# Kernel optimization log

Hardware: AMD Instinct MI355X
Metric: run time of the kernel (lower is better)

## Reference

```python
import jax, jax.numpy as jnp
import numpy as np

L, C, H = 4, 512, 8
HD = C // H

def silu(x):
    return x * jax.nn.sigmoid(x)

def layernorm(x, g, b, eps=1e-5):
    m = x.mean(-1, keepdims=True)
    v = ((x - m) ** 2).mean(-1, keepdims=True)
    return (x - m) * jax.lax.rsqrt(v + eps) * g + b

def adaln(x, t, w, b):
    # x: (N,B,C), t: (B,C), w: (2C,C), b: (2C,)
    mod = silu(t) @ w.T + b
    scale, shift = jnp.split(mod, 2, axis=-1)
    return x * (1.0 + scale[None]) + shift[None]

def embed_rotary(x, pos):
    # x: (B,N,C), pos: (B,N,C,2) with [...,0]=cos, [...,1]=sin
    cos, sin = pos[..., 0], pos[..., 1]
    x2 = jnp.stack([-x[..., 1::2], x[..., 0::2]], axis=-1).reshape(x.shape)
    return x * cos + x2 * sin

def setup_inputs() -> dict:
    key = jax.random.key(0)
    ks = jax.random.split(key, 24)
    Nq, Nkv, B = 1024, 2048, 4
    query = jax.random.normal(ks[0], (Nq, B, C), jnp.float32)
    value = jax.random.normal(ks[1], (Nkv, B, C), jnp.float32)
    diff_ts = jax.random.normal(ks[2], (B, C), jnp.float32)
    # valid rotary codes: cos/sin of random angles
    aq = jax.random.uniform(ks[3], (B, Nq, C), jnp.float32, 0.0, 2 * np.pi)
    ak = jax.random.uniform(ks[4], (B, Nkv, C), jnp.float32, 0.0, 2 * np.pi)
    query_pos = jnp.stack([jnp.cos(aq), jnp.sin(aq)], axis=-1)
    value_pos = jnp.stack([jnp.cos(ak), jnp.sin(ak)], axis=-1)
    s = 0.02
    inp = dict(query=query, value=value, diff_ts=diff_ts,
               query_pos=query_pos, value_pos=value_pos,
               aw_attn=jax.random.normal(ks[5], (L, 2 * C, C)) * s,
               ab_attn=jax.random.normal(ks[6], (L, 2 * C)) * s,
               in_w=jax.random.normal(ks[7], (L, 3 * C, C)) * s,
               in_b=jnp.zeros((L, 3 * C)),
               out_w=jax.random.normal(ks[8], (L, C, C)) * s,
               out_b=jnp.zeros((L, C)),
               ln1_g=jnp.ones((L, C)), ln1_b=jnp.zeros((L, C)),
               aw_ffn=jax.random.normal(ks[9], (L, 2 * C, C)) * s,
               ab_ffn=jax.random.normal(ks[10], (L, 2 * C)) * s,
               w1=jax.random.normal(ks[11], (L, C, C)) * s,
               b1=jnp.zeros((L, C)),
               w2=jax.random.normal(ks[12], (L, C, C)) * s,
               b2=jnp.zeros((L, C)),
               ln2_g=jnp.ones((L, C)), ln2_b=jnp.zeros((L, C)))
    return inp

def _forward(query, value, diff_ts, query_pos, value_pos,
             aw_attn, ab_attn, in_w, in_b, out_w, out_b, ln1_g, ln1_b,
             aw_ffn, ab_ffn, w1, b1, w2, b2, ln2_g, ln2_b):
    Nq, B, _ = query.shape
    Nkv = value.shape[0]
    scaling = HD ** -0.5
    outputs = []
    q = query
    for i in range(L):
        # --- cross-attention layer ---
        aq = adaln(q, diff_ts, aw_attn[i], ab_attn[i])
        wq, wk, wv = jnp.split(in_w[i], 3, axis=0)
        bq, bk, bv = jnp.split(in_b[i], 3, axis=0)
        qp = (aq @ wq.T + bq) * scaling          # (Nq,B,C)
        kp = value @ wk.T + bk                    # (Nkv,B,C)
        vp = value @ wv.T + bv
        qb = embed_rotary(qp.transpose(1, 0, 2), query_pos)  # (B,Nq,C)
        kb = embed_rotary(kp.transpose(1, 0, 2), value_pos)  # (B,Nkv,C)
        vb = vp.transpose(1, 0, 2)
        qh = qb.reshape(B, Nq, H, HD).transpose(0, 2, 1, 3)   # (B,H,Nq,HD)
        kh = kb.reshape(B, Nkv, H, HD).transpose(0, 2, 1, 3)
        vh = vb.reshape(B, Nkv, H, HD).transpose(0, 2, 1, 3)
        scores = jnp.einsum('bhqd,bhkd->bhqk', qh, kh)
        attn = jax.nn.softmax(scores, axis=-1)
        o = jnp.einsum('bhqk,bhkd->bhqd', attn, vh)
        o = o.transpose(0, 2, 1, 3).reshape(B, Nq, C).transpose(1, 0, 2)  # (Nq,B,C)
        o = o @ out_w[i].T + out_b[i]
        q = layernorm(q + o, ln1_g[i], ln1_b[i])
        # --- feedforward layer (residual uses AdaLN-modulated x) ---
        xa = adaln(q, diff_ts, aw_ffn[i], ab_ffn[i])
        h = jax.nn.relu(xa @ w1[i].T + b1[i])
        h = h @ w2[i].T + b2[i]
        q = layernorm(xa + h, ln2_g[i], ln2_b[i])
        outputs.append(q)
    return jnp.stack(outputs)  # (L, Nq, B, C)

def reference(query, value, diff_ts, query_pos, value_pos,
              aw_attn, ab_attn, in_w, in_b, out_w, out_b, ln1_g, ln1_b,
              aw_ffn, ab_ffn, w1, b1, w2, b2, ln2_g, ln2_b):
    return _forward(query, value, diff_ts, query_pos, value_pos,
                    aw_attn, ab_attn, in_w, in_b, out_w, out_b, ln1_g, ln1_b,
                    aw_ffn, ab_ffn, w1, b1, w2, b2, ln2_g, ln2_b)
```

## Files before the change

### kernel.cpp

```cpp
#include <hip/hip_runtime.h>
#include <hip/hip_bf16.h>

typedef __hip_bfloat16 bf16;
typedef __attribute__((ext_vector_type(8))) short short8;
typedef __attribute__((ext_vector_type(4))) short s16x4;
typedef __attribute__((ext_vector_type(4))) float f32x4;

#define CDIM 512
#define BDIM 4
#define HDIM 8
#define HDQ  64
#define NQ   1024
#define NKV  2048
#define LAYERS 4
#define SPLIT 2

#if defined(__has_builtin)
#if __has_builtin(__builtin_amdgcn_global_load_lds)
#define USE_GLL 1
#endif
#endif

static __device__ __forceinline__ short f2s(float f) {
    bf16 h = __float2bfloat16(f);
    return *reinterpret_cast<short*>(&h);
}


__global__ __launch_bounds__(256) void convall_k(
    const float* __restrict__ s0, const float* __restrict__ s1,
    const float* __restrict__ s2, const float* __restrict__ s3,
    const float* __restrict__ s4,
    bf16* __restrict__ d0, bf16* __restrict__ d1, bf16* __restrict__ d2,
    bf16* __restrict__ d3, bf16* __restrict__ d4) {
    int gid = blockIdx.x * 256 + threadIdx.x;
    const float* src; bf16* dst; int off;
    if (gid < 1048576)      { src = s0; dst = d0; off = gid; }
    else if (gid < 1835008) { src = s1; dst = d1; off = gid - 1048576; }
    else if (gid < 2097152) { src = s2; dst = d2; off = gid - 1835008; }
    else if (gid < 2359296) { src = s3; dst = d3; off = gid - 2097152; }
    else                    { src = s4; dst = d4; off = gid - 2359296; }
    f32x4 v = *(const f32x4*)(src + (size_t)off * 4);
    s16x4 o;
    o[0] = f2s(v[0]); o[1] = f2s(v[1]); o[2] = f2s(v[2]); o[3] = f2s(v[3]);
    *(s16x4*)(dst + (size_t)off * 4) = o;
}

__global__ __launch_bounds__(256) void modall_k(const float* __restrict__ diff_ts,
    const float* __restrict__ aw_attn, const float* __restrict__ ab_attn,
    const float* __restrict__ aw_ffn,  const float* __restrict__ ab_ffn,
    float* __restrict__ mod) {
    int wv = blockIdx.x * 4 + (threadIdx.x >> 6);
    int lane = threadIdx.x & 63;
    int col  = wv & 1023;
    int b    = (wv >> 10) & 3;
    int kind = (wv >> 12) & 1;
    int l    = wv >> 13;
    const float* w = (kind ? aw_ffn : aw_attn) + ((size_t)l * 1024 + col) * CDIM + lane * 8;
    const float* tb = diff_ts + b * CDIM + lane * 8;
    f32x4 w0 = *(const f32x4*)w;
    f32x4 w1 = *(const f32x4*)(w + 4);
    f32x4 t0 = *(const f32x4*)tb;
    f32x4 t1 = *(const f32x4*)(tb + 4);
    #pragma unroll
    for (int j = 0; j < 4; ++j) {
        t0[j] = t0[j] / (1.f + __expf(-t0[j]));
        t1[j] = t1[j] / (1.f + __expf(-t1[j]));
    }
    f32x4 pp = w0 * t0 + w1 * t1;
    float acc = (pp[0] + pp[1]) + (pp[2] + pp[3]);
    #pragma unroll
    for (int off = 32; off; off >>= 1) acc += __shfl_xor(acc, off);
    if (lane == 0)
        mod[wv] = acc + (kind ? ab_ffn : ab_attn)[l * 1024 + col];
}

__global__ __launch_bounds__(256) void adaln_k(const float* __restrict__ x,
                                               const float* __restrict__ mod,
                                               bf16* __restrict__ outb) {
    int i = blockIdx.x * 256 + threadIdx.x;
    int c = i & 511;
    int b = (i >> 9) & 3;
    outb[i] = __float2bfloat16(x[i] * (1.f + mod[b * 1024 + c]) + mod[b * 1024 + 512 + c]);
}

__global__ __launch_bounds__(256) void ln_ad_k(const float* __restrict__ x,
                                               const float* __restrict__ res,
                                               const float* __restrict__ g,
                                               const float* __restrict__ bb,
                                               const float* __restrict__ mod,
                                               float* __restrict__ ln_f,
                                               float* __restrict__ ln_f2,
                                               float* __restrict__ ad_f,
                                               bf16* __restrict__ ad_b) {
    int row = blockIdx.x;
    int t = threadIdx.x;
    size_t base = (size_t)row * CDIM;
    float v0 = x[base + t] + res[base + t];
    float v1 = x[base + t + 256] + res[base + t + 256];
    float s1 = v0 + v1;
    float s2 = v0 * v0 + v1 * v1;
    #pragma unroll
    for (int off = 32; off; off >>= 1) {
        s1 += __shfl_xor(s1, off);
        s2 += __shfl_xor(s2, off);
    }
    __shared__ float a1[4], a2[4];
    int w = t >> 6;
    if ((t & 63) == 0) { a1[w] = s1; a2[w] = s2; }
    __syncthreads();
    s1 = a1[0] + a1[1] + a1[2] + a1[3];
    s2 = a2[0] + a2[1] + a2[2] + a2[3];
    float mean = s1 * (1.f / 512.f);
    float var = s2 * (1.f / 512.f) - mean * mean;
    float rs = rsqrtf(var + 1e-5f);
    float y0 = (v0 - mean) * rs * g[t] + bb[t];
    float y1 = (v1 - mean) * rs * g[t + 256] + bb[t + 256];
    if (ln_f)  { ln_f[base + t] = y0;  ln_f[base + t + 256] = y1; }
    if (ln_f2) { ln_f2[base + t] = y0; ln_f2[base + t + 256] = y1; }
    if (mod) {
        int b = row & 3;
        float o0 = y0 * (1.f + mod[b * 1024 + t]) + mod[b * 1024 + 512 + t];
        float o1 = y1 * (1.f + mod[b * 1024 + t + 256]) + mod[b * 1024 + 512 + t + 256];
        if (ad_f) { ad_f[base + t] = o0; ad_f[base + t + 256] = o1; }
        ad_b[base + t] = __float2bfloat16(o0);
        ad_b[base + t + 256] = __float2bfloat16(o1);
    }
}

template <int EPI, int WM, int NT>
__global__ __launch_bounds__(256) void mgemm_k(
    const bf16* __restrict__ A, const bf16* __restrict__ Wt,
    const float* __restrict__ bias, void* __restrict__ out0v,
    void* __restrict__ out1v, int M, int N, int K,
    const float* __restrict__ pos, float scl, int Nseq) {
    __shared__ bf16 As[2][2][64 * 32];
    __shared__ bf16 Bs[2][2][64 * 32];
    int t = threadIdx.x;
    int w = t >> 6;
    int lane = t & 63;
    int l16 = lane & 15;
    int quad = lane >> 4;
    int wy = w >> 1, wx = w & 1;
    int bm = blockIdx.y * 64;
    int bn = blockIdx.x * 64;
    int lr2 = lane >> 2;
    int lc4 = lane & 3;

    f32x4 acc[WM][NT] = {};

    auto stage = [&](int buf, int k0) {
#if USE_GLL
        const bf16* sa = A + (size_t)(bm + w * 16 + lr2) * K + k0 + lc4 * 8;
        const bf16* sb = Wt + (size_t)(bn + w * 16 + lr2) * K + k0 + lc4 * 8;
        #pragma unroll
        for (int j = 0; j < 2; ++j) {
            __builtin_amdgcn_global_load_lds(
                (const unsigned int __attribute__((address_space(1)))*)(sa + j * 32),
                (unsigned int __attribute__((address_space(3)))*)(&As[buf][j][w * 512]),
                16, 0, 0);
            __builtin_amdgcn_global_load_lds(
                (const unsigned int __attribute__((address_space(1)))*)(sb + j * 32),
                (unsigned int __attribute__((address_space(3)))*)(&Bs[buf][j][w * 512]),
                16, 0, 0);
        }
#else
        for (int e = t; e < 512; e += 256) {
            int sub = e >> 8, c = e & 255;
            int row = c >> 2, c4 = c & 3;
            *(uint4*)&As[buf][sub][row * 32 + c4 * 8] =
                *(const uint4*)(A + (size_t)(bm + row) * K + k0 + sub * 32 + c4 * 8);
            *(uint4*)&Bs[buf][sub][row * 32 + c4 * 8] =
                *(const uint4*)(Wt + (size_t)(bn + row) * K + k0 + sub * 32 + c4 * 8);
        }
#endif
    };

    stage(0, 0);
    __syncthreads();
    int cur = 0;

    for (int k0 = 0; k0 < K; k0 += 64) {
        if (k0 + 64 < K) stage(cur ^ 1, k0 + 64);

        #pragma unroll
        for (int kk = 0; kk < 2; ++kk) {
            short8 af[WM], bfr[NT];
            #pragma unroll
            for (int mt = 0; mt < WM; ++mt)
                af[mt] = *(const short8*)
                    &As[cur][kk][((wy * WM + mt) * 16 + l16) * 32 + quad * 8];
            #pragma unroll
            for (int nt = 0; nt < NT; ++nt)
                bfr[nt] = *(const short8*)
                    &Bs[cur][kk][((wx * NT + nt) * 16 + l16) * 32 + quad * 8];
            #pragma unroll
            for (int mt = 0; mt < WM; ++mt)
                #pragma unroll
                for (int nt = 0; nt < NT; ++nt)
                    acc[mt][nt] = __builtin_amdgcn_mfma_f32_16x16x32_bf16(
                        af[mt], bfr[nt], acc[mt][nt], 0, 0, 0);
        }

        __syncthreads();
        cur ^= 1;
    }

    #pragma unroll
    for (int nt = 0; nt < NT; ++nt) {
        int n = bn + (wx * NT + nt) * 16 + l16;
        float bnv = (EPI == 4) ? 0.f : bias[n];
        #pragma unroll
        for (int mt = 0; mt < WM; ++mt) {
            #pragma unroll
            for (int r = 0; r < 4; ++r) {
                int m = bm + (wy * WM + mt) * 16 + quad * 4 + r;
                float v = acc[mt][nt][r] + ((EPI == 4) ? bias[m] : bnv);
                if (EPI == 0) {
                    ((float*)out0v)[(size_t)m * N + n] = v;
                } else if (EPI == 1) {
                    ((bf16*)out0v)[(size_t)m * N + n] = __float2bfloat16(fmaxf(v, 0.f));
                } else if (EPI == 4) {
                    int hh = m >> 6, dd = m & 63;
                    int bsel = n & 3, key = n >> 2;
                    ((bf16*)out0v)[((size_t)(bsel * HDIM + hh) * HDQ + dd) * NKV + key] =
                        __float2bfloat16(v);
                } else {
                    v *= scl;
                    int c = n;
                    int nseq = m >> 2, b = m & 3;
                    float part = __shfl_xor(v, 1);
                    const float* pp = pos + (((size_t)b * Nseq + nseq) * CDIM + c) * 2;
                    float cs = pp[0], sn = pp[1];
                    float o = (l16 & 1) ? (v * cs + part * sn) : (v * cs - part * sn);
                    bf16* op = (bf16*)out0v +
                               ((size_t)(b * HDIM + (c >> 6)) * Nseq + nseq) * HDQ + (c & 63);
                    *op = __float2bfloat16(o);
                }
            }
        }
    }
}

__global__ __launch_bounds__(256) void attn4_k(const bf16* __restrict__ qh,
                                               const bf16* __restrict__ kh,
                                               const bf16* __restrict__ vT,
                                               float* __restrict__ pl,
                                               float* __restrict__ pacc) {
    __shared__ short Kb[2][64 * 64];
    __shared__ short Vb[2][64 * 64];
    __shared__ short Ps[4][16 * 64];
    int t = threadIdx.x;
    int wave = t >> 6, lane = t & 63;
    int l16 = lane & 15, quad = lane >> 4;
    int bh = blockIdx.y;
    int q0 = blockIdx.x * 64 + wave * 16;
    int kbase = blockIdx.z * (NKV / SPLIT);

    const bf16* qbase = qh + ((size_t)bh * NQ + q0) * HDQ;
    short8 aq0 = *(const short8*)(qbase + (size_t)l16 * HDQ + quad * 8);
    short8 aq1 = *(const short8*)(qbase + (size_t)l16 * HDQ + 32 + quad * 8);
    const bf16* kbh = kh + ((size_t)bh * NKV + kbase) * HDQ;
    const bf16* vbh = vT + (size_t)bh * HDQ * NKV + kbase;

    int r0 = wave * 16;
    int lr = lane >> 3;
    int swz_src = ((lane & 7) ^ lr) * 8;

    auto stage = [&](int buf, int kt) {
#if USE_GLL
        #pragma unroll
        for (int j = 0; j < 2; ++j) {
            int rr = r0 + j * 8;
            __builtin_amdgcn_global_load_lds(
                (const unsigned int __attribute__((address_space(1)))*)
                    (kbh + (size_t)(kt + rr + lr) * HDQ + swz_src),
                (unsigned int __attribute__((address_space(3)))*)&Kb[buf][rr * 64],
                16, 0, 0);
            __builtin_amdgcn_global_load_lds(
                (const unsigned int __attribute__((address_space(1)))*)
                    (vbh + (size_t)(rr + lr) * NKV + kt + swz_src),
                (unsigned int __attribute__((address_space(3)))*)&Vb[buf][rr * 64],
                16, 0, 0);
        }
#else
        #pragma unroll
        for (int j = 0; j < 2; ++j) {
            int rr = r0 + j * 8 + lr;
            int lc = lane & 7;
            *(short8*)&Kb[buf][rr * 64 + ((lc ^ (rr & 7)) * 8)] =
                *(const short8*)(kbh + (size_t)(kt + rr) * HDQ + lc * 8);
            *(short8*)&Vb[buf][rr * 64 + ((lc ^ (rr & 7)) * 8)] =
                *(const short8*)(vbh + (size_t)rr * NKV + kt + lc * 8);
        }
#endif
    };

    f32x4 accO[4] = {};
    float lsum[4] = {0.f, 0.f, 0.f, 0.f};

    stage(0, 0);
    __syncthreads();
    int cur = 0;
    int swz_m = l16 & 7;

    for (int kt = 0; kt < NKV / SPLIT; kt += 64) {
        if (kt + 64 < NKV / SPLIT) stage(cur ^ 1, kt + 64);

        f32x4 sc[4] = {};
        #pragma unroll
        for (int nt = 0; nt < 4; ++nt) {
            const short* kr = &Kb[cur][(nt * 16 + l16) * 64];
            short8 bk0 = *(const short8*)&kr[(quad ^ swz_m) * 8];
            short8 bk1 = *(const short8*)&kr[((quad + 4) ^ swz_m) * 8];
            sc[nt] = __builtin_amdgcn_mfma_f32_16x16x32_bf16(aq0, bk0, sc[nt], 0, 0, 0);
            sc[nt] = __builtin_amdgcn_mfma_f32_16x16x32_bf16(aq1, bk1, sc[nt], 0, 0, 0);
        }

        #pragma unroll
        for (int r = 0; r < 4; ++r) {
            float p0 = exp2f(sc[0][r]);
            float p1 = exp2f(sc[1][r]);
            float p2 = exp2f(sc[2][r]);
            float p3 = exp2f(sc[3][r]);
            lsum[r] += (p0 + p1) + (p2 + p3);
            int pr = quad * 4 + r;
            short* prow = &Ps[wave][pr * 64];
            int pm = pr & 7;
            int ch = l16 >> 3, kl = l16 & 7;
            prow[((ch ^ pm) << 3) + kl]       = f2s(p0);
            prow[(((ch + 2) ^ pm) << 3) + kl] = f2s(p1);
            prow[(((ch + 4) ^ pm) << 3) + kl] = f2s(p2);
            prow[(((ch + 6) ^ pm) << 3) + kl] = f2s(p3);
        }

        const short* prd = &Ps[wave][l16 * 64];
        short8 pa0 = *(const short8*)&prd[(quad ^ swz_m) * 8];
        short8 pa1 = *(const short8*)&prd[((quad + 4) ^ swz_m) * 8];
        #pragma unroll
        for (int nt = 0; nt < 4; ++nt) {
            const short* vr = &Vb[cur][(nt * 16 + l16) * 64];
            short8 bv0 = *(const short8*)&vr[(quad ^ swz_m) * 8];
            short8 bv1 = *(const short8*)&vr[((quad + 4) ^ swz_m) * 8];
            accO[nt] = __builtin_amdgcn_mfma_f32_16x16x32_bf16(pa0, bv0, accO[nt], 0, 0, 0);
            accO[nt] = __builtin_amdgcn_mfma_f32_16x16x32_bf16(pa1, bv1, accO[nt], 0, 0, 0);
        }

        __syncthreads();
        cur ^= 1;
    }

    #pragma unroll
    for (int r = 0; r < 4; ++r) {
        #pragma unroll
        for (int off = 1; off < 16; off <<= 1) lsum[r] += __shfl_xor(lsum[r], off);
    }

    size_t rowbase = ((size_t)blockIdx.z * 32 + bh) * NQ + q0;
    #pragma unroll
    for (int r = 0; r < 4; ++r) {
        size_t row = rowbase + quad * 4 + r;
        if (l16 == 0) pl[row] = lsum[r];
        #pragma unroll
        for (int nt = 0; nt < 4; ++nt)
            pacc[row * 64 + nt * 16 + l16] = accO[nt][r];
    }
}

__global__ __launch_bounds__(256) void attn_comb_k(const float* __restrict__ pl,
                                                   const float* __restrict__ pacc,
                                                   bf16* __restrict__ o) {
    int idx = blockIdx.x * 256 + threadIdx.x;
    int d = idx & 63;
    int row = idx >> 6;
    int q = row & (NQ - 1);
    int bh = row >> 10;
    const int S = 32 * NQ;
    float l = pl[row] + pl[S + row];
    float v = pacc[(size_t)row * 64 + d] + pacc[(size_t)(S + row) * 64 + d];
    int b = bh >> 3, h = bh & 7;
    o[((size_t)(q * BDIM + b)) * CDIM + h * HDQ + d] = __float2bfloat16(v / l);
}


extern "C" void kernel_launch(void* const* d_in, const int* in_sizes, int n_in,
                              void* d_out, int out_size, void* d_ws, size_t ws_size,
                              hipStream_t stream) {
    const float* query     = (const float*)d_in[0];
    const float* value     = (const float*)d_in[1];
    const float* diff_ts   = (const float*)d_in[2];
    const float* query_pos = (const float*)d_in[3];
    const float* value_pos = (const float*)d_in[4];
    const float* aw_attn   = (const float*)d_in[5];
    const float* ab_attn   = (const float*)d_in[6];
    const float* in_w      = (const float*)d_in[7];
    const float* in_b      = (const float*)d_in[8];
    const float* out_w     = (const float*)d_in[9];
    const float* out_b     = (const float*)d_in[10];
    const float* ln1_g     = (const float*)d_in[11];
    const float* ln1_b     = (const float*)d_in[12];
    const float* aw_ffn    = (const float*)d_in[13];
    const float* ab_ffn    = (const float*)d_in[14];
    const float* w1        = (const float*)d_in[15];
    const float* b1        = (const float*)d_in[16];
    const float* w2        = (const float*)d_in[17];
    const float* b2        = (const float*)d_in[18];
    const float* ln2_g     = (const float*)d_in[19];
    const float* ln2_b     = (const float*)d_in[20];
    float* out_f = (float*)d_out;

    float* ws      = (float*)d_ws;
    float* mod_ws  = ws + 2048;
    float* q_cur   = ws + 34816;
    float* buf_a   = q_cur + 2097152;
    float* buf_p   = buf_a + 2097152;
    bf16* a_bf     = (bf16*)(buf_p + 2097152);
    bf16* h_bf     = a_bf + 2097152;
    bf16* qh       = h_bf + 2097152;
    bf16* kh       = qh + 2097152;
    bf16* vt       = kh + 4194304;
    bf16* val_bf   = vt + 4194304;
    bf16* winb     = val_bf + 4194304;
    bf16* woutb    = winb + 3145728;
    bf16* w1b      = woutb + 1048576;
    bf16* w2b      = w1b + 1048576;
    float* pacc    = buf_a;
    float* pl      = (float*)a_bf;

    const int MQ = NQ * BDIM;
    const int MKV = NKV * BDIM;
    const float scaling = 0.125f * 1.44269504f;

    modall_k<<<8192, 256, 0, stream>>>(diff_ts, aw_attn, ab_attn, aw_ffn, ab_ffn, mod_ws);
    convall_k<<<10240, 256, 0, stream>>>(value, in_w, out_w, w1, w2,
                                         val_bf, winb, woutb, w1b, w2b);
    adaln_k<<<(MQ * CDIM) / 256, 256, 0, stream>>>(query, mod_ws, a_bf);

    for (int i = 0; i < LAYERS; ++i) {
        const float* mod_ffn  = mod_ws + i * 8192 + 4096;
        const float* mod_attn_next = (i + 1 < LAYERS) ? (mod_ws + (i + 1) * 8192) : nullptr;
        const bf16* winb_i = winb + (size_t)i * 1536 * CDIM;
        const float* in_b_i = in_b + (size_t)i * 1536;
        const float* qsrc = (i == 0) ? query : q_cur;

        mgemm_k<2, 2, 2><<<dim3(8, MQ / 64), 256, 0, stream>>>(
            a_bf, winb_i, in_b_i, qh, nullptr, MQ, 512, CDIM, query_pos, scaling, NQ);
        mgemm_k<2, 2, 2><<<dim3(8, MKV / 64), 256, 0, stream>>>(
            val_bf, winb_i + (size_t)512 * CDIM, in_b_i + 512, kh, nullptr, MKV, 512,
            CDIM, value_pos, 1.f, NKV);
        mgemm_k<4, 2, 2><<<dim3(MKV / 64, 8), 256, 0, stream>>>(
            winb_i + (size_t)1024 * CDIM, val_bf, in_b_i + 1024, vt, nullptr,
            512, MKV, CDIM, nullptr, 0.f, 0);
        attn4_k<<<dim3(NQ / 64, BDIM * HDIM, SPLIT), 256, 0, stream>>>(
            qh, kh, vt, pl, pacc);
        attn_comb_k<<<8192, 256, 0, stream>>>(pl, pacc, h_bf);
        mgemm_k<0, 2, 2><<<dim3(8, MQ / 64), 256, 0, stream>>>(
            h_bf, woutb + (size_t)i * CDIM * CDIM, out_b + i * CDIM, buf_p, nullptr,
            MQ, 512, CDIM, nullptr, 0.f, 0);
        ln_ad_k<<<MQ, 256, 0, stream>>>(qsrc, buf_p, ln1_g + i * CDIM, ln1_b + i * CDIM,
                                        mod_ffn, nullptr, nullptr, buf_a, a_bf);
        mgemm_k<1, 2, 2><<<dim3(8, MQ / 64), 256, 0, stream>>>(
            a_bf, w1b + (size_t)i * CDIM * CDIM, b1 + i * CDIM, h_bf, nullptr,
            MQ, 512, CDIM, nullptr, 0.f, 0);
        mgemm_k<0, 2, 2><<<dim3(8, MQ / 64), 256, 0, stream>>>(
            h_bf, w2b + (size_t)i * CDIM * CDIM, b2 + i * CDIM, buf_p, nullptr,
            MQ, 512, CDIM, nullptr, 0.f, 0);
        ln_ad_k<<<MQ, 256, 0, stream>>>(buf_a, buf_p, ln2_g + i * CDIM, ln2_b + i * CDIM,
                                        mod_attn_next, q_cur,
                                        out_f + (size_t)i * MQ * CDIM, nullptr, a_bf);
    }
}
```

Measured before the change: 701.5 us.

## Merge QKV projections into one launch, split-K small GEMMs, remap attention grid

The three Q/K/V projection GEMMs become one kernel that picks its section from the block index, which removes two launches and fills the GPU with one larger grid. The out-projection and FFN2 GEMMs are split along K into two partial outputs, doubling the block count for these 512-block GEMMs. The partial sums are added inside the following layernorm kernel. The attention grid is flattened and its block ids permuted, plausibly to spread work across XCDs and improve cache locality. The split-K costs an extra fp32 partial buffer write and read.

```diff
diff --git a/kernel.cpp b/kernel.cpp
--- a/kernel.cpp
+++ b/kernel.cpp
@@ -86,6 +86,7 @@
 
 __global__ __launch_bounds__(256) void ln_ad_k(const float* __restrict__ x,
                                                const float* __restrict__ res,
+                                               const float* __restrict__ res2,
                                                const float* __restrict__ g,
                                                const float* __restrict__ bb,
                                                const float* __restrict__ mod,
@@ -98,6 +99,10 @@
     size_t base = (size_t)row * CDIM;
     float v0 = x[base + t] + res[base + t];
     float v1 = x[base + t + 256] + res[base + t + 256];
+    if (res2) {
+        v0 += res2[base + t];
+        v1 += res2[base + t + 256];
+    }
     float s1 = v0 + v1;
     float s2 = v0 * v0 + v1 * v1;
     #pragma unroll
@@ -128,7 +133,7 @@
     }
 }
 
-template <int EPI, int WM, int NT>
+template <int EPI, int WM, int NT, int KS>
 __global__ __launch_bounds__(256) void mgemm_k(
     const bf16* __restrict__ A, const bf16* __restrict__ Wt,
     const float* __restrict__ bias, void* __restrict__ out0v,
@@ -147,6 +152,9 @@
     int lr2 = lane >> 2;
     int lc4 = lane & 3;
 
+    int kbeg = 0, kend = K;
+    if (KS == 2) { int half = K >> 1; kbeg = blockIdx.z * half; kend = kbeg + half; }
+
     f32x4 acc[WM][NT] = {};
 
     auto stage = [&](int buf, int k0) {
@@ -176,12 +184,12 @@
 #endif
     };
 
-    stage(0, 0);
+    stage(0, kbeg);
     __syncthreads();
     int cur = 0;
 
-    for (int k0 = 0; k0 < K; k0 += 64) {
-        if (k0 + 64 < K) stage(cur ^ 1, k0 + 64);
+    for (int k0 = kbeg; k0 < kend; k0 += 64) {
+        if (k0 + 64 < kend) stage(cur ^ 1, k0 + 64);
 
         #pragma unroll
         for (int kk = 0; kk < 2; ++kk) {
@@ -206,24 +214,141 @@
         cur ^= 1;
     }
 
+    float* fout = (KS == 2 && blockIdx.z) ? (float*)out1v : (float*)out0v;
     #pragma unroll
     for (int nt = 0; nt < NT; ++nt) {
         int n = bn + (wx * NT + nt) * 16 + l16;
-        float bnv = (EPI == 4) ? 0.f : bias[n];
+        float bnv = (KS == 2 && blockIdx.z) ? 0.f : bias[n];
         #pragma unroll
         for (int mt = 0; mt < WM; ++mt) {
             #pragma unroll
             for (int r = 0; r < 4; ++r) {
                 int m = bm + (wy * WM + mt) * 16 + quad * 4 + r;
-                float v = acc[mt][nt][r] + ((EPI == 4) ? bias[m] : bnv);
+                float v = acc[mt][nt][r] + bnv;
                 if (EPI == 0) {
-                    ((float*)out0v)[(size_t)m * N + n] = v;
-                } else if (EPI == 1) {
+                    fout[(size_t)m * N + n] = v;
+                } else {
                     ((bf16*)out0v)[(size_t)m * N + n] = __float2bfloat16(fmaxf(v, 0.f));
-                } else if (EPI == 4) {
+                }
+            }
+        }
+    }
+}
+
+__global__ __launch_bounds__(256) void qkv_k(
+    const bf16* __restrict__ winb_i, const float* __restrict__ in_b_i,
+    const bf16* __restrict__ a_bf, const bf16* __restrict__ val_bf,
+    bf16* __restrict__ qh, bf16* __restrict__ kh, bf16* __restrict__ vt,
+    const float* __restrict__ qpos, const float* __restrict__ vpos,
+    float scaling) {
+    __shared__ bf16 As[2][2][64 * 32];
+    __shared__ bf16 Bs[2][2][64 * 32];
+    int bx = blockIdx.x;
+    int sec, bm, bn;
+    const bf16 *A, *Wt;
+    const float* bias;
+    const float* pos = nullptr;
+    bf16* out;
+    float scl = 1.f;
+    int Nseq = 0;
+    if (bx < 512) {
+        sec = 0; bn = bx & 7; bm = bx >> 3;
+        A = a_bf; Wt = winb_i; bias = in_b_i; out = qh;
+        pos = qpos; scl = scaling; Nseq = NQ;
+    } else if (bx < 1536) {
+        sec = 1; int i2 = bx - 512; bn = i2 & 7; bm = i2 >> 3;
+        A = val_bf; Wt = winb_i + (size_t)512 * CDIM; bias = in_b_i + 512;
+        out = kh; pos = vpos; scl = 1.f; Nseq = NKV;
+    } else {
+        sec = 2; int i2 = bx - 1536; bm = i2 & 7; bn = i2 >> 3;
+        A = winb_i + (size_t)1024 * CDIM; Wt = val_bf; bias = in_b_i + 1024;
+        out = vt;
+    }
+    bm *= 64; bn *= 64;
+    const int K = CDIM;
+
+    int t = threadIdx.x;
+    int w = t >> 6;
+    int lane = t & 63;
+    int l16 = lane & 15;
+    int quad = lane >> 4;
+    int wy = w >> 1, wx = w & 1;
+    int lr2 = lane >> 2;
+    int lc4 = lane & 3;
+
+    f32x4 acc[2][2] = {};
+
+    auto stage = [&](int buf, int k0) {
+#if USE_GLL
+        const bf16* sa = A + (size_t)(bm + w * 16 + lr2) * K + k0 + lc4 * 8;
+        const bf16* sb = Wt + (size_t)(bn + w * 16 + lr2) * K + k0 + lc4 * 8;
+        #pragma unroll
+        for (int j = 0; j < 2; ++j) {
+            __builtin_amdgcn_global_load_lds(
+                (const unsigned int __attribute__((address_space(1)))*)(sa + j * 32),
+                (unsigned int __attribute__((address_space(3)))*)(&As[buf][j][w * 512]),
+                16, 0, 0);
+            __builtin_amdgcn_global_load_lds(
+                (const unsigned int __attribute__((address_space(1)))*)(sb + j * 32),
+                (unsigned int __attribute__((address_space(3)))*)(&Bs[buf][j][w * 512]),
+                16, 0, 0);
+        }
+#else
+        for (int e = t; e < 512; e += 256) {
+            int sub = e >> 8, c = e & 255;
+            int row = c >> 2, c4 = c & 3;
+            *(uint4*)&As[buf][sub][row * 32 + c4 * 8] =
+                *(const uint4*)(A + (size_t)(bm + row) * K + k0 + sub * 32 + c4 * 8);
+            *(uint4*)&Bs[buf][sub][row * 32 + c4 * 8] =
+                *(const uint4*)(Wt + (size_t)(bn + row) * K + k0 + sub * 32 + c4 * 8);
+        }
+#endif
+    };
+
+    stage(0, 0);
+    __syncthreads();
+    int cur = 0;
+
+    for (int k0 = 0; k0 < K; k0 += 64) {
+        if (k0 + 64 < K) stage(cur ^ 1, k0 + 64);
+
+        #pragma unroll
+        for (int kk = 0; kk < 2; ++kk) {
+            short8 af[2], bfr[2];
+            #pragma unroll
+            for (int mt = 0; mt < 2; ++mt)
+                af[mt] = *(const short8*)
+                    &As[cur][kk][((wy * 2 + mt) * 16 + l16) * 32 + quad * 8];
+            #pragma unroll
+            for (int nt = 0; nt < 2; ++nt)
+                bfr[nt] = *(const short8*)
+                    &Bs[cur][kk][((wx * 2 + nt) * 16 + l16) * 32 + quad * 8];
+            #pragma unroll
+            for (int mt = 0; mt < 2; ++mt)
+                #pragma unroll
+                for (int nt = 0; nt < 2; ++nt)
+                    acc[mt][nt] = __builtin_amdgcn_mfma_f32_16x16x32_bf16(
+                        af[mt], bfr[nt], acc[mt][nt], 0, 0, 0);
+        }
+
+        __syncthreads();
+        cur ^= 1;
+    }
+
+    #pragma unroll
+    for (int nt = 0; nt < 2; ++nt) {
+        int n = bn + (wx * 2 + nt) * 16 + l16;
+        float bnv = (sec == 2) ? 0.f : bias[n];
+        #pragma unroll
+        for (int mt = 0; mt < 2; ++mt) {
+            #pragma unroll
+            for (int r = 0; r < 4; ++r) {
+                int m = bm + (wy * 2 + mt) * 16 + quad * 4 + r;
+                float v = acc[mt][nt][r] + ((sec == 2) ? bias[m] : bnv);
+                if (sec == 2) {
                     int hh = m >> 6, dd = m & 63;
                     int bsel = n & 3, key = n >> 2;
-                    ((bf16*)out0v)[((size_t)(bsel * HDIM + hh) * HDQ + dd) * NKV + key] =
+                    vt[((size_t)(bsel * HDIM + hh) * HDQ + dd) * NKV + key] =
                         __float2bfloat16(v);
                 } else {
                     v *= scl;
@@ -233,7 +358,7 @@
                     const float* pp = pos + (((size_t)b * Nseq + nseq) * CDIM + c) * 2;
                     float cs = pp[0], sn = pp[1];
                     float o = (l16 & 1) ? (v * cs + part * sn) : (v * cs - part * sn);
-                    bf16* op = (bf16*)out0v +
+                    bf16* op = out +
                                ((size_t)(b * HDIM + (c >> 6)) * Nseq + nseq) * HDQ + (c & 63);
                     *op = __float2bfloat16(o);
                 }
@@ -253,9 +378,15 @@
     int t = threadIdx.x;
     int wave = t >> 6, lane = t & 63;
     int l16 = lane & 15, quad = lane >> 4;
-    int bh = blockIdx.y;
-    int q0 = blockIdx.x * 64 + wave * 16;
-    int kbase = blockIdx.z * (NKV / SPLIT);
+
+    int b0 = blockIdx.x;
+    int newid = (b0 & 7) * 128 + (b0 >> 3);
+    int qtile = newid & 15;
+    int grp = newid >> 4;
+    int split = grp & 1;
+    int bh = grp >> 1;
+    int q0 = qtile * 64 + wave * 16;
+    int kbase = split * (NKV / SPLIT);
 
     const bf16* qbase = qh + ((size_t)bh * NQ + q0) * HDQ;
     short8 aq0 = *(const short8*)(qbase + (size_t)l16 * HDQ + quad * 8);
@@ -356,7 +487,7 @@
         for (int off = 1; off < 16; off <<= 1) lsum[r] += __shfl_xor(lsum[r], off);
     }
 
-    size_t rowbase = ((size_t)blockIdx.z * 32 + bh) * NQ + q0;
+    size_t rowbase = ((size_t)split * 32 + bh) * NQ + q0;
     #pragma unroll
     for (int r = 0; r < 4; ++r) {
         size_t row = rowbase + quad * 4 + r;
@@ -424,11 +555,11 @@
     bf16* woutb    = winb + 3145728;
     bf16* w1b      = woutb + 1048576;
     bf16* w2b      = w1b + 1048576;
+    float* buf_p2  = (float*)(w2b + 1048576);
     float* pacc    = buf_a;
     float* pl      = (float*)a_bf;
 
     const int MQ = NQ * BDIM;
-    const int MKV = NKV * BDIM;
     const float scaling = 0.125f * 1.44269504f;
 
     modall_k<<<8192, 256, 0, stream>>>(diff_ts, aw_attn, ab_attn, aw_ffn, ab_ffn, mod_ws);
@@ -443,29 +574,24 @@
         const float* in_b_i = in_b + (size_t)i * 1536;
         const float* qsrc = (i == 0) ? query : q_cur;
 
-        mgemm_k<2, 2, 2><<<dim3(8, MQ / 64), 256, 0, stream>>>(
-            a_bf, winb_i, in_b_i, qh, nullptr, MQ, 512, CDIM, query_pos, scaling, NQ);
-        mgemm_k<2, 2, 2><<<dim3(8, MKV / 64), 256, 0, stream>>>(
-            val_bf, winb_i + (size_t)512 * CDIM, in_b_i + 512, kh, nullptr, MKV, 512,
-            CDIM, value_pos, 1.f, NKV);
-        mgemm_k<4, 2, 2><<<dim3(MKV / 64, 8), 256, 0, stream>>>(
-            winb_i + (size_t)1024 * CDIM, val_bf, in_b_i + 1024, vt, nullptr,
-            512, MKV, CDIM, nullptr, 0.f, 0);
-        attn4_k<<<dim3(NQ / 64, BDIM * HDIM, SPLIT), 256, 0, stream>>>(
-            qh, kh, vt, pl, pacc);
+        qkv_k<<<2560, 256, 0, stream>>>(winb_i, in_b_i, a_bf, val_bf,
+                                        qh, kh, vt, query_pos, value_pos, scaling);
+        attn4_k<<<1024, 256, 0, stream>>>(qh, kh, vt, pl, pacc);
         attn_comb_k<<<8192, 256, 0, stream>>>(pl, pacc, h_bf);
-        mgemm_k<0, 2, 2><<<dim3(8, MQ / 64), 256, 0, stream>>>(
-            h_bf, woutb + (size_t)i * CDIM * CDIM, out_b + i * CDIM, buf_p, nullptr,
+        mgemm_k<0, 2, 2, 2><<<dim3(8, MQ / 64, 2), 256, 0, stream>>>(
+            h_bf, woutb + (size_t)i * CDIM * CDIM, out_b + i * CDIM, buf_p, buf_p2,
             MQ, 512, CDIM, nullptr, 0.f, 0);
-        ln_ad_k<<<MQ, 256, 0, stream>>>(qsrc, buf_p, ln1_g + i * CDIM, ln1_b + i * CDIM,
+        ln_ad_k<<<MQ, 256, 0, stream>>>(qsrc, buf_p, buf_p2,
+                                        ln1_g + i * CDIM, ln1_b + i * CDIM,
                                         mod_ffn, nullptr, nullptr, buf_a, a_bf);
-        mgemm_k<1, 2, 2><<<dim3(8, MQ / 64), 256, 0, stream>>>(
+        mgemm_k<1, 2, 2, 1><<<dim3(8, MQ / 64), 256, 0, stream>>>(
             a_bf, w1b + (size_t)i * CDIM * CDIM, b1 + i * CDIM, h_bf, nullptr,
             MQ, 512, CDIM, nullptr, 0.f, 0);
-        mgemm_k<0, 2, 2><<<dim3(8, MQ / 64), 256, 0, stream>>>(
-            h_bf, w2b + (size_t)i * CDIM * CDIM, b2 + i * CDIM, buf_p, nullptr,
+        mgemm_k<0, 2, 2, 2><<<dim3(8, MQ / 64, 2), 256, 0, stream>>>(
+            h_bf, w2b + (size_t)i * CDIM * CDIM, b2 + i * CDIM, buf_p, buf_p2,
             MQ, 512, CDIM, nullptr, 0.f, 0);
-        ln_ad_k<<<MQ, 256, 0, stream>>>(buf_a, buf_p, ln2_g + i * CDIM, ln2_b + i * CDIM,
+        ln_ad_k<<<MQ, 256, 0, stream>>>(buf_a, buf_p, buf_p2,
+                                        ln2_g + i * CDIM, ln2_b + i * CDIM,
                                         mod_attn_next, q_cur,
                                         out_f + (size_t)i * MQ * CDIM, nullptr, a_bf);
     }
```

Result: slower. 748.1 us (+6.6%).

## Add split-K GEMMs, XCD-aware block swizzle, and LDS bank-conflict XOR swizzle

Applied to the files above, without the earlier changes.

Makes the out-proj and FFN2 GEMMs split-K by two, writing partial sums to a second buffer that the following layernorm kernel adds in. This doubles block count for those small-N GEMMs. Block IDs in the GEMMs and the attention kernel are remapped so consecutive blocks spread across the 8 XCDs, aiming at better L2 locality. The LDS tile layout is XOR-swizzled on load and read to reduce bank conflicts. The cost is extra partial-sum traffic and an extra read in layernorm.

```diff
diff --git a/kernel.cpp b/kernel.cpp
--- a/kernel.cpp
+++ b/kernel.cpp
@@ -86,6 +86,7 @@
 
 __global__ __launch_bounds__(256) void ln_ad_k(const float* __restrict__ x,
                                                const float* __restrict__ res,
+                                               const float* __restrict__ res2,
                                                const float* __restrict__ g,
                                                const float* __restrict__ bb,
                                                const float* __restrict__ mod,
@@ -98,6 +99,10 @@
     size_t base = (size_t)row * CDIM;
     float v0 = x[base + t] + res[base + t];
     float v1 = x[base + t + 256] + res[base + t + 256];
+    if (res2) {
+        v0 += res2[base + t];
+        v1 += res2[base + t + 256];
+    }
     float s1 = v0 + v1;
     float s2 = v0 * v0 + v1 * v1;
     #pragma unroll
@@ -128,7 +133,7 @@
     }
 }
 
-template <int EPI, int WM, int NT>
+template <int EPI, int WM, int NT, int KS, bool SWZ>
 __global__ __launch_bounds__(256) void mgemm_k(
     const bf16* __restrict__ A, const bf16* __restrict__ Wt,
     const float* __restrict__ bias, void* __restrict__ out0v,
@@ -142,10 +147,25 @@
     int l16 = lane & 15;
     int quad = lane >> 4;
     int wy = w >> 1, wx = w & 1;
-    int bm = blockIdx.y * 64;
-    int bn = blockIdx.x * 64;
+
+    int bxi, byi, bzi;
+    if (SWZ) {
+        int nx = gridDim.x, ny = gridDim.y;
+        int flat = (blockIdx.z * ny + blockIdx.y) * nx + blockIdx.x;
+        int nwg = nx * ny * gridDim.z;
+        int s = (flat & 7) * (nwg >> 3) + (flat >> 3);
+        bxi = s % nx; int rest = s / nx; byi = rest % ny; bzi = rest / ny;
+    } else {
+        bxi = blockIdx.x; byi = blockIdx.y; bzi = blockIdx.z;
+    }
+    int bm = byi * 64;
+    int bn = bxi * 64;
+
     int lr2 = lane >> 2;
-    int lc4 = lane & 3;
+    int lc4 = (lane & 3) ^ ((lane >> 3) & 3);
+
+    int kbeg = 0, kend = K;
+    if (KS == 2) { int half = K >> 1; kbeg = bzi * half; kend = kbeg + half; }
 
     f32x4 acc[WM][NT] = {};
 
@@ -168,20 +188,22 @@
         for (int e = t; e < 512; e += 256) {
             int sub = e >> 8, c = e & 255;
             int row = c >> 2, c4 = c & 3;
+            int srcc = c4 ^ ((row >> 1) & 3);
             *(uint4*)&As[buf][sub][row * 32 + c4 * 8] =
-                *(const uint4*)(A + (size_t)(bm + row) * K + k0 + sub * 32 + c4 * 8);
+                *(const uint4*)(A + (size_t)(bm + row) * K + k0 + sub * 32 + srcc * 8);
             *(uint4*)&Bs[buf][sub][row * 32 + c4 * 8] =
-                *(const uint4*)(Wt + (size_t)(bn + row) * K + k0 + sub * 32 + c4 * 8);
+                *(const uint4*)(Wt + (size_t)(bn + row) * K + k0 + sub * 32 + srcc * 8);
         }
 #endif
     };
 
-    stage(0, 0);
+    stage(0, kbeg);
     __syncthreads();
     int cur = 0;
-
-    for (int k0 = 0; k0 < K; k0 += 64) {
-        if (k0 + 64 < K) stage(cur ^ 1, k0 + 64);
+    int rchunk = (quad ^ ((l16 >> 1) & 3)) * 8;
+
+    for (int k0 = kbeg; k0 < kend; k0 += 64) {
+        if (k0 + 64 < kend) stage(cur ^ 1, k0 + 64);
 
         #pragma unroll
         for (int kk = 0; kk < 2; ++kk) {
@@ -189,11 +211,11 @@
             #pragma unroll
             for (int mt = 0; mt < WM; ++mt)
                 af[mt] = *(const short8*)
-                    &As[cur][kk][((wy * WM + mt) * 16 + l16) * 32 + quad * 8];
+                    &As[cur][kk][((wy * WM + mt) * 16 + l16) * 32 + rchunk];
             #pragma unroll
             for (int nt = 0; nt < NT; ++nt)
                 bfr[nt] = *(const short8*)
-                    &Bs[cur][kk][((wx * NT + nt) * 16 + l16) * 32 + quad * 8];
+                    &Bs[cur][kk][((wx * NT + nt) * 16 + l16) * 32 + rchunk];
             #pragma unroll
             for (int mt = 0; mt < WM; ++mt)
                 #pragma unroll
@@ -206,10 +228,11 @@
         cur ^= 1;
     }
 
+    float* fout = (KS == 2 && bzi) ? (float*)out1v : (float*)out0v;
     #pragma unroll
     for (int nt = 0; nt < NT; ++nt) {
         int n = bn + (wx * NT + nt) * 16 + l16;
-        float bnv = (EPI == 4) ? 0.f : bias[n];
+        float bnv = (EPI == 4 || (KS == 2 && bzi)) ? 0.f : bias[n];
         #pragma unroll
         for (int mt = 0; mt < WM; ++mt) {
             #pragma unroll
@@ -217,7 +240,7 @@
                 int m = bm + (wy * WM + mt) * 16 + quad * 4 + r;
                 float v = acc[mt][nt][r] + ((EPI == 4) ? bias[m] : bnv);
                 if (EPI == 0) {
-                    ((float*)out0v)[(size_t)m * N + n] = v;
+                    fout[(size_t)m * N + n] = v;
                 } else if (EPI == 1) {
                     ((bf16*)out0v)[(size_t)m * N + n] = __float2bfloat16(fmaxf(v, 0.f));
                 } else if (EPI == 4) {
@@ -253,9 +276,15 @@
     int t = threadIdx.x;
     int wave = t >> 6, lane = t & 63;
     int l16 = lane & 15, quad = lane >> 4;
-    int bh = blockIdx.y;
-    int q0 = blockIdx.x * 64 + wave * 16;
-    int kbase = blockIdx.z * (NKV / SPLIT);
+
+    int b0 = blockIdx.x;
+    int newid = (b0 & 7) * 128 + (b0 >> 3);
+    int qtile = newid & 15;
+    int grp = newid >> 4;
+    int split = grp & 1;
+    int bh = grp >> 1;
+    int q0 = qtile * 64 + wave * 16;
+    int kbase = split * (NKV / SPLIT);
 
     const bf16* qbase = qh + ((size_t)bh * NQ + q0) * HDQ;
     short8 aq0 = *(const short8*)(qbase + (size_t)l16 * HDQ + quad * 8);
@@ -356,7 +385,7 @@
         for (int off = 1; off < 16; off <<= 1) lsum[r] += __shfl_xor(lsum[r], off);
     }
 
-    size_t rowbase = ((size_t)blockIdx.z * 32 + bh) * NQ + q0;
+    size_t rowbase = ((size_t)split * 32 + bh) * NQ + q0;
     #pragma unroll
     for (int r = 0; r < 4; ++r) {
         size_t row = rowbase + quad * 4 + r;
@@ -424,6 +453,7 @@
     bf16* woutb    = winb + 3145728;
     bf16* w1b      = woutb + 1048576;
     bf16* w2b      = w1b + 1048576;
+    float* buf_p2  = (float*)(w2b + 1048576);
     float* pacc    = buf_a;
     float* pl      = (float*)a_bf;
 
@@ -443,29 +473,30 @@
         const float* in_b_i = in_b + (size_t)i * 1536;
         const float* qsrc = (i == 0) ? query : q_cur;
 
-        mgemm_k<2, 2, 2><<<dim3(8, MQ / 64), 256, 0, stream>>>(
+        mgemm_k<2, 2, 2, 1, true><<<dim3(8, MQ / 64), 256, 0, stream>>>(
             a_bf, winb_i, in_b_i, qh, nullptr, MQ, 512, CDIM, query_pos, scaling, NQ);
-        mgemm_k<2, 2, 2><<<dim3(8, MKV / 64), 256, 0, stream>>>(
+        mgemm_k<2, 2, 2, 1, true><<<dim3(8, MKV / 64), 256, 0, stream>>>(
             val_bf, winb_i + (size_t)512 * CDIM, in_b_i + 512, kh, nullptr, MKV, 512,
             CDIM, value_pos, 1.f, NKV);
-        mgemm_k<4, 2, 2><<<dim3(MKV / 64, 8), 256, 0, stream>>>(
+        mgemm_k<4, 2, 2, 1, false><<<dim3(MKV / 64, 8), 256, 0, stream>>>(
             winb_i + (size_t)1024 * CDIM, val_bf, in_b_i + 1024, vt, nullptr,
             512, MKV, CDIM, nullptr, 0.f, 0);
-        attn4_k<<<dim3(NQ / 64, BDIM * HDIM, SPLIT), 256, 0, stream>>>(
-            qh, kh, vt, pl, pacc);
+        attn4_k<<<1024, 256, 0, stream>>>(qh, kh, vt, pl, pacc);
         attn_comb_k<<<8192, 256, 0, stream>>>(pl, pacc, h_bf);
-        mgemm_k<0, 2, 2><<<dim3(8, MQ / 64), 256, 0, stream>>>(
-            h_bf, woutb + (size_t)i * CDIM * CDIM, out_b + i * CDIM, buf_p, nullptr,
+        mgemm_k<0, 2, 2, 2, true><<<dim3(8, MQ / 64, 2), 256, 0, stream>>>(
+            h_bf, woutb + (size_t)i * CDIM * CDIM, out_b + i * CDIM, buf_p, buf_p2,
             MQ, 512, CDIM, nullptr, 0.f, 0);
-        ln_ad_k<<<MQ, 256, 0, stream>>>(qsrc, buf_p, ln1_g + i * CDIM, ln1_b + i * CDIM,
+        ln_ad_k<<<MQ, 256, 0, stream>>>(qsrc, buf_p, buf_p2,
+                                        ln1_g + i * CDIM, ln1_b + i * CDIM,
                                         mod_ffn, nullptr, nullptr, buf_a, a_bf);
-        mgemm_k<1, 2, 2><<<dim3(8, MQ / 64), 256, 0, stream>>>(
+        mgemm_k<1, 2, 2, 1, true><<<dim3(8, MQ / 64), 256, 0, stream>>>(
             a_bf, w1b + (size_t)i * CDIM * CDIM, b1 + i * CDIM, h_bf, nullptr,
             MQ, 512, CDIM, nullptr, 0.f, 0);
-        mgemm_k<0, 2, 2><<<dim3(8, MQ / 64), 256, 0, stream>>>(
-            h_bf, w2b + (size_t)i * CDIM * CDIM, b2 + i * CDIM, buf_p, nullptr,
+        mgemm_k<0, 2, 2, 2, true><<<dim3(8, MQ / 64, 2), 256, 0, stream>>>(
+            h_bf, w2b + (size_t)i * CDIM * CDIM, b2 + i * CDIM, buf_p, buf_p2,
             MQ, 512, CDIM, nullptr, 0.f, 0);
-        ln_ad_k<<<MQ, 256, 0, stream>>>(buf_a, buf_p, ln2_g + i * CDIM, ln2_b + i * CDIM,
+        ln_ad_k<<<MQ, 256, 0, stream>>>(buf_a, buf_p, buf_p2,
+                                        ln2_g + i * CDIM, ln2_b + i * CDIM,
                                         mod_attn_next, q_cur,
                                         out_f + (size_t)i * MQ * CDIM, nullptr, a_bf);
     }
```

Measured after the change: 709.3 us. About the same (+1.1%).
